# Performance work log

Measured on AMD Instinct MI355X. Metric: run time of the kernel, lower is better.

Reference implementation:

```python
import jax, jax.numpy as jnp
import numpy as np


def setup_inputs() -> dict:
    key = jax.random.key(0)
    tensor = jax.random.uniform(key, (8192, 64, 64), dtype=jnp.float32)
    return {"tensor": tensor}


def reference(tensor):
    # tensor: [B, H, W]
    B, H, W = tensor.shape
    # argmax per batch (first occurrence, matching the torch scan order)
    flat_idx = jnp.argmax(tensor.reshape(B, H * W), axis=1)  # [B]
    max_x = flat_idx // W  # row index of max, [B]
    max_y = flat_idx % W   # col index of max, [B]
    j = jnp.arange(H)
    k = jnp.arange(W)
    # squared distance from each (j,k) to the per-batch argmax location: [B,H,W]
    dist2 = ((max_x[:, None, None] - j[None, :, None]) ** 2
             + (max_y[:, None, None] - k[None, None, :]) ** 2)
    loss = jnp.sum(dist2.astype(tensor.dtype) * tensor)
    return loss.reshape(1)
```

## Files before the change

### kernel.cpp

```cpp
#include <hip/hip_runtime.h>


#define NB   8192
#define HW   4096
#define TPB  256
#define VPT  4

__global__ __launch_bounds__(TPB) void loss_main_kernel(
    const float* __restrict__ in, float* __restrict__ partial) {
    const int b = blockIdx.x;
    const int t = threadIdx.x;
    const int wave = t >> 6;
    const int lane = t & 63;

    const float4* base = (const float4*)(in + (size_t)b * HW);

    float4 v[VPT];
#pragma unroll
    for (int i = 0; i < VPT; ++i) {
        v[i] = base[i * TPB + t];
    }

    float best = -1.0f;
    int bidx = 0;
#pragma unroll
    for (int i = 0; i < VPT; ++i) {
        const int fi = (i * TPB + t) * 4;
        const float vals[4] = {v[i].x, v[i].y, v[i].z, v[i].w};
#pragma unroll
        for (int c = 0; c < 4; ++c) {
            if (vals[c] > best) { best = vals[c]; bidx = fi + c; }
        }
    }

#pragma unroll
    for (int off = 32; off > 0; off >>= 1) {
        float oval = __shfl_down(best, off, 64);
        int   oidx = __shfl_down(bidx, off, 64);
        if (oval > best || (oval == best && oidx < bidx)) { best = oval; bidx = oidx; }
    }

    __shared__ float sval[4];
    __shared__ int   sidx[4];
    __shared__ int   smxy;
    if (lane == 0) { sval[wave] = best; sidx[wave] = bidx; }
    __syncthreads();
    if (t == 0) {
        float bb = sval[0]; int bi = sidx[0];
#pragma unroll
        for (int w = 1; w < 4; ++w) {
            if (sval[w] > bb || (sval[w] == bb && sidx[w] < bi)) { bb = sval[w]; bi = sidx[w]; }
        }
        smxy = bi;
    }
    __syncthreads();
    const float mx = (float)(smxy >> 6);
    const float my = (float)(smxy & 63);

    float acc = 0.0f;
#pragma unroll
    for (int i = 0; i < VPT; ++i) {
        const int fi = (i * TPB + t) * 4;
        const float vals[4] = {v[i].x, v[i].y, v[i].z, v[i].w};
        const float dj = mx - (float)(fi >> 6);
        const float dj2 = dj * dj;
        const float kbase = (float)(fi & 63);
#pragma unroll
        for (int c = 0; c < 4; ++c) {
            const float dk = my - (kbase + (float)c);
            acc += (dj2 + dk * dk) * vals[c];
        }
    }

#pragma unroll
    for (int off = 32; off > 0; off >>= 1) acc += __shfl_down(acc, off, 64);
    __shared__ float ssum[4];
    if (lane == 0) ssum[wave] = acc;
    __syncthreads();
    if (t == 0) partial[b] = ssum[0] + ssum[1] + ssum[2] + ssum[3];
}

__global__ __launch_bounds__(TPB) void loss_reduce_kernel(
    const float* __restrict__ partial, float* __restrict__ out) {
    const int t = threadIdx.x;
    float acc = 0.0f;
#pragma unroll
    for (int i = 0; i < NB / TPB; ++i) acc += partial[i * TPB + t];
#pragma unroll
    for (int off = 32; off > 0; off >>= 1) acc += __shfl_down(acc, off, 64);
    __shared__ float s[4];
    const int wave = t >> 6, lane = t & 63;
    if (lane == 0) s[wave] = acc;
    __syncthreads();
    if (t == 0) out[0] = s[0] + s[1] + s[2] + s[3];
}

extern "C" void kernel_launch(void* const* d_in, const int* in_sizes, int n_in,
                              void* d_out, int out_size, void* d_ws, size_t ws_size,
                              hipStream_t stream) {
    const float* in = (const float*)d_in[0];
    float* out = (float*)d_out;
    float* partial = (float*)d_ws;

    loss_main_kernel<<<NB, TPB, 0, stream>>>(in, partial);
    loss_reduce_kernel<<<1, TPB, 0, stream>>>(partial, out);
}
```

Baseline: 185.3 us.

## Expand squared distance into moment sums to eliminate second pass and barrier

Rewrites the per-batch loss as (mx²+my²)·S − 2mx·Sj − 2my·Sk + Sd, where S, Sj, Sk and Sd are moments accumulated in the same pass as the argmax. This removes the second barrier, the broadcast of the argmax location, and the second sweep over register values, at the cost of four extra shuffle reductions. The reduce kernel also switches to float4 loads. The expanded form subtracts large terms from each other in fp32, which may hurt accuracy through cancellation.

```diff
diff --git a/kernel.cpp b/kernel.cpp
--- a/kernel.cpp
+++ b/kernel.cpp
@@ -17,82 +17,79 @@
 
     float4 v[VPT];
 #pragma unroll
-    for (int i = 0; i < VPT; ++i) {
-        v[i] = base[i * TPB + t];
-    }
+    for (int i = 0; i < VPT; ++i) v[i] = base[i * TPB + t];
 
-    float best = -1.0f;
-    int bidx = 0;
+    float S = 0.f, Sj = 0.f, Sk = 0.f, Sd = 0.f;
+    float best = -1.f;
+    int   bidx = 0;
 #pragma unroll
     for (int i = 0; i < VPT; ++i) {
         const int fi = (i * TPB + t) * 4;
+        const float fj  = (float)(fi >> 6);
+        const float fj2 = fj * fj;
+        const float kb  = (float)(fi & 63);
         const float vals[4] = {v[i].x, v[i].y, v[i].z, v[i].w};
 #pragma unroll
         for (int c = 0; c < 4; ++c) {
-            if (vals[c] > best) { best = vals[c]; bidx = fi + c; }
+            const float val = vals[c];
+            const float fk  = kb + (float)c;
+            S  += val;
+            Sj  = fmaf(fj, val, Sj);
+            Sk  = fmaf(fk, val, Sk);
+            Sd  = fmaf(fj2 + fk * fk, val, Sd);
+            if (val > best) { best = val; bidx = fi + c; }
         }
     }
 
 #pragma unroll
     for (int off = 32; off > 0; off >>= 1) {
-        float oval = __shfl_down(best, off, 64);
-        int   oidx = __shfl_down(bidx, off, 64);
+        S  += __shfl_down(S,  off, 64);
+        Sj += __shfl_down(Sj, off, 64);
+        Sk += __shfl_down(Sk, off, 64);
+        Sd += __shfl_down(Sd, off, 64);
+        const float oval = __shfl_down(best, off, 64);
+        const int   oidx = __shfl_down(bidx, off, 64);
         if (oval > best || (oval == best && oidx < bidx)) { best = oval; bidx = oidx; }
     }
 
-    __shared__ float sval[4];
-    __shared__ int   sidx[4];
-    __shared__ int   smxy;
-    if (lane == 0) { sval[wave] = best; sidx[wave] = bidx; }
+    __shared__ float sS[4], sSj[4], sSk[4], sSd[4], sBest[4];
+    __shared__ int   sIdx[4];
+    if (lane == 0) {
+        sS[wave] = S; sSj[wave] = Sj; sSk[wave] = Sk; sSd[wave] = Sd;
+        sBest[wave] = best; sIdx[wave] = bidx;
+    }
     __syncthreads();
     if (t == 0) {
-        float bb = sval[0]; int bi = sidx[0];
+        float tS = sS[0], tSj = sSj[0], tSk = sSk[0], tSd = sSd[0];
+        float bb = sBest[0]; int bi = sIdx[0];
 #pragma unroll
         for (int w = 1; w < 4; ++w) {
-            if (sval[w] > bb || (sval[w] == bb && sidx[w] < bi)) { bb = sval[w]; bi = sidx[w]; }
+            tS += sS[w]; tSj += sSj[w]; tSk += sSk[w]; tSd += sSd[w];
+            if (sBest[w] > bb || (sBest[w] == bb && sIdx[w] < bi)) { bb = sBest[w]; bi = sIdx[w]; }
         }
-        smxy = bi;
+        const float mx = (float)(bi >> 6);
+        const float my = (float)(bi & 63);
+        partial[b] = (mx * mx + my * my) * tS - 2.f * mx * tSj - 2.f * my * tSk + tSd;
     }
-    __syncthreads();
-    const float mx = (float)(smxy >> 6);
-    const float my = (float)(smxy & 63);
-
-    float acc = 0.0f;
-#pragma unroll
-    for (int i = 0; i < VPT; ++i) {
-        const int fi = (i * TPB + t) * 4;
-        const float vals[4] = {v[i].x, v[i].y, v[i].z, v[i].w};
-        const float dj = mx - (float)(fi >> 6);
-        const float dj2 = dj * dj;
-        const float kbase = (float)(fi & 63);
-#pragma unroll
-        for (int c = 0; c < 4; ++c) {
-            const float dk = my - (kbase + (float)c);
-            acc += (dj2 + dk * dk) * vals[c];
-        }
-    }
-
-#pragma unroll
-    for (int off = 32; off > 0; off >>= 1) acc += __shfl_down(acc, off, 64);
-    __shared__ float ssum[4];
-    if (lane == 0) ssum[wave] = acc;
-    __syncthreads();
-    if (t == 0) partial[b] = ssum[0] + ssum[1] + ssum[2] + ssum[3];
 }
 
 __global__ __launch_bounds__(TPB) void loss_reduce_kernel(
     const float* __restrict__ partial, float* __restrict__ out) {
     const int t = threadIdx.x;
+    const float4* p4 = (const float4*)partial;
     float acc = 0.0f;
 #pragma unroll
-    for (int i = 0; i < NB / TPB; ++i) acc += partial[i * TPB + t];
+    for (int i = 0; i < NB / (TPB * 4); ++i) {
+        const float4 p = p4[i * TPB + t];
+        acc += (p.x + p.y) + (p.z + p.w);
+    }
 #pragma unroll
     for (int off = 32; off > 0; off >>= 1) acc += __shfl_down(acc, off, 64);
     __shared__ float s[4];
     const int wave = t >> 6, lane = t & 63;
     if (lane == 0) s[wave] = acc;
     __syncthreads();
-    if (t == 0) out[0] = s[0] + s[1] + s[2] + s[3];
+    if (t == 0) out[0] = (s[0] + s[1]) + (s[2] + s[3]);
 }
 
 extern "C" void kernel_launch(void* const* d_in, const int* in_sizes, int n_in,
```

Measured after the change: 185.8 us. About the same (+0.3%).
